# Optimization experiments

Hardware: AMD Instinct MI355X
Metric: run time of the kernel (lower is better)

## Reference

```python
import jax, jax.numpy as jnp
import numpy as np

WS = 8          # window_size
SHIFT = WS // 2 # shift for 'SW' type
HEADS = 6
HD = 32


def setup_inputs() -> dict:
    key = jax.random.key(0)
    ks = jax.random.split(key, 6)
    return {
        "x": jax.random.normal(ks[0], (4, 256, 256, 192), jnp.float32),
        "w_qkv": jax.random.normal(ks[1], (192, 576), jnp.float32) * 0.02,
        "b_qkv": jax.random.normal(ks[2], (576,), jnp.float32) * 0.02,
        "rel_pos": jax.random.normal(ks[3], (HEADS, 2 * WS - 1, 2 * WS - 1), jnp.float32) * 0.02,
        "w_out": jax.random.normal(ks[4], (192, 192), jnp.float32) * 0.02,
        "b_out": jax.random.normal(ks[5], (192,), jnp.float32) * 0.02,
    }


def reference(x, w_qkv, b_qkv, rel_pos, w_out, b_out):
    b, h, w, c = x.shape
    scale = HD ** (-0.5)
    wa = WS * WS  # window area
    # shifted-window roll
    x = jnp.roll(x, (-SHIFT, -SHIFT), axis=(1, 2))
    hw, ww = h // WS, w // WS
    nw = hw * ww
    # partition into windows: [b, nw, wa, c]
    xw = x.reshape(b, hw, WS, ww, WS, c).transpose(0, 1, 3, 2, 4, 5).reshape(b, nw, wa, c)
    qkv = xw @ w_qkv + b_qkv                       # [b, nw, wa, 3c]
    qkv = qkv.reshape(b, nw, wa, 3, HEADS, HD)
    q = qkv[..., 0, :, :] * scale
    k = qkv[..., 1, :, :]
    v = qkv[..., 2, :, :]
    attn = jnp.einsum('bnqhd,bnkhd->bnhqk', q, k)  # [b, nw, heads, wa, wa]
    # relative position bias
    coords = jnp.stack(jnp.meshgrid(jnp.arange(WS), jnp.arange(WS), indexing='ij')).reshape(2, -1).T  # [wa,2]
    rel = coords[:, None, :] - coords[None, :, :] + WS - 1   # [wa, wa, 2]
    bias = rel_pos[:, rel[..., 0], rel[..., 1]]              # [heads, wa, wa]
    attn = attn + bias[None, None]
    # shift mask (only last window masked, per the module's generate_mask)
    s = WS - SHIFT
    mask = jnp.zeros((nw, wa, wa), bool)
    mask = mask.at[-1, :s, s:].set(True).at[-1, s:, :s].set(True)
    attn = jnp.where(mask[None, :, None], -jnp.inf, attn)
    attn = jax.nn.softmax(attn, axis=-1)
    out = jnp.einsum('bnhqk,bnkhd->bnqhd', attn, v)          # [b, nw, wa, heads, hd]
    out = out.reshape(b, hw, ww, WS, WS, c).transpose(0, 1, 3, 2, 4, 5).reshape(b, h, w, c)
    out = out @ w_out + b_out
    out = jnp.roll(out, (SHIFT, SHIFT), axis=(1, 2))
    return out
```

## Files before the change

### kernel.cpp

```cpp
#include <hip/hip_runtime.h>
#include <hip/hip_bf16.h>

typedef __attribute__((ext_vector_type(8))) short short8;
typedef __attribute__((ext_vector_type(4))) float f32x4;
typedef __attribute__((ext_vector_type(4))) unsigned short u16x4;

#define MFMA(a, b, c) __builtin_amdgcn_mfma_f32_16x16x32_bf16((a), (b), (c), 0, 0, 0)

namespace {
constexpr int IMG = 256;
constexpr int NWIN = 1024;
constexpr float SCALE = 0.17677669529663687f;
constexpr float L2E   = 1.4426950408889634f;
}

__device__ __forceinline__ unsigned short f2bf1(float f) {
    __hip_bfloat16 h = __float2bfloat16(f);
    union { __hip_bfloat16 h; unsigned short u; } v; v.h = h;
    return v.u;
}
__device__ __forceinline__ unsigned pack2(float a, float b) {
    __hip_bfloat162 h = __float22bfloat162_rn(make_float2(a, b));
    union { __hip_bfloat162 h; unsigned u; } v; v.h = h;
    return v.u;
}
__device__ __forceinline__ float bf2f(unsigned short h) {
    union { unsigned u; float f; } v; v.u = ((unsigned)h) << 16;
    return v.f;
}

__global__ __launch_bounds__(256) void to_bf16_T(const float* __restrict__ in,
                                                 unsigned short* __restrict__ out,
                                                 int K, int N, int scale_n, float scale) {
    __shared__ float tile[32][65];
    const int t = threadIdx.x;
    const int nb = blockIdx.x * 64, kb = blockIdx.y * 32;
    const int tn = t & 63, tk = t >> 6;
#pragma unroll
    for (int p = 0; p < 8; ++p)
        tile[p * 4 + tk][tn] = in[(size_t)(kb + p * 4 + tk) * N + nb + tn];
    __syncthreads();
    const int n = t >> 2, kc = (t & 3) * 8;
    const float s = (nb + n) < scale_n ? scale : 1.0f;
    uint4 u;
    u.x = pack2(tile[kc + 0][n] * s, tile[kc + 1][n] * s);
    u.y = pack2(tile[kc + 2][n] * s, tile[kc + 3][n] * s);
    u.z = pack2(tile[kc + 4][n] * s, tile[kc + 5][n] * s);
    u.w = pack2(tile[kc + 6][n] * s, tile[kc + 7][n] * s);
    *(uint4*)(out + (size_t)(nb + n) * K + kb + kc) = u;
}

__global__ __launch_bounds__(256) void build_bias(const float* __restrict__ rel_pos,
                                                  const float* __restrict__ b_qkv,
                                                  unsigned short* __restrict__ bias3,
                                                  float* __restrict__ bq2) {
    const int o = blockIdx.x * 256 + threadIdx.x;
    const int k = o & 63, q = (o >> 6) & 63, h = o >> 12;
    const int qy = q >> 3, qx = q & 7, ky = k >> 3, kx = k & 7;
    const float bv = rel_pos[h * 225 + (qy - ky + 7) * 15 + (qx - kx + 7)] * L2E;
    bias3[o] = f2bf1(bv);
    const bool masked = (q < 4) != (k < 4);
    bias3[24576 + o] = masked ? f2bf1(-30000.0f) : f2bf1(bv);
    if (blockIdx.x == 0) {
        for (int i = threadIdx.x; i < 576; i += 256)
            bq2[i] = b_qkv[i] * (i < 192 ? SCALE : 1.0f);
    }
}

__global__ __launch_bounds__(256, 3)
void qkv_attn(const float* __restrict__ x,
              const float* __restrict__ bq2,
              const unsigned short* __restrict__ bias3,
              const unsigned short* __restrict__ wqT,
              unsigned short* __restrict__ oh_ws) {
    __shared__ unsigned short x_s[64][200];
    __shared__ unsigned short qp_s[64][72];
    __shared__ unsigned short kp_s[64][72];
    __shared__ unsigned short vT_s[64][72];

    const int tid = threadIdx.x;
    const int w   = tid >> 6;
    const int l   = tid & 63;
    const int l15 = l & 15, lg = l >> 4;
    const int wing = blockIdx.x;
    const int b   = wing >> 10;
    const int win = wing & (NWIN - 1);
    const int wy  = win >> 5, wx = win & 31;
    const unsigned short* bias_t = bias3 + ((win == NWIN - 1) ? 24576 : 0);

    {
        int t = tid / 48, r = tid % 48;
#pragma unroll
        for (int it = 0; it < 12; ++it) {
            const int pr = ((wy << 3) + (t >> 3) + 4) & (IMG - 1);
            const int pc = ((wx << 3) + (t & 7) + 4) & (IMG - 1);
            const float4 xv = *reinterpret_cast<const float4*>(
                x + ((size_t)((b * IMG + pr) * IMG + pc)) * 192 + r * 4);
            uint2 pk; pk.x = pack2(xv.x, xv.y); pk.y = pack2(xv.z, xv.w);
            *(uint2*)(&x_s[t][r * 4]) = pk;
            r += 16; t += 5;
            if (r >= 48) { r -= 48; t += 1; }
        }
    }
    __syncthreads();

    const int h_loc = w >> 1;
    const int qt0   = 2 * (w & 1);

#pragma unroll 1
    for (int g = 0; g < 3; ++g) {
        f32x4 aq[3][4];
#pragma unroll
        for (int ci = 0; ci < 3; ++ci) {
            const int t = w + 4 * ci;
            const int which = t >> 2, sub = t & 3;
            const int hh = sub >> 1, d0 = (sub & 1) * 16;
            f32x4 c0;
            if (which < 2) {
                const float4 b4 = *reinterpret_cast<const float4*>(
                    bq2 + which * 192 + (2 * g + hh) * 32 + d0 + 4 * lg);
                c0 = f32x4{b4.x, b4.y, b4.z, b4.w};
            } else {
                const float bb = bq2[384 + (2 * g + hh) * 32 + d0 + l15];
                c0 = f32x4{bb, bb, bb, bb};
            }
#pragma unroll
            for (int nt = 0; nt < 4; ++nt) aq[ci][nt] = c0;
        }

        __builtin_amdgcn_s_setprio(1);
#pragma unroll
        for (int ks = 0; ks < 6; ++ks) {
            short8 xf[4];
#pragma unroll
            for (int nt = 0; nt < 4; ++nt)
                xf[nt] = *(const short8*)(&x_s[16 * nt + l15][ks * 32 + lg * 8]);
#pragma unroll
            for (int ci = 0; ci < 3; ++ci) {
                const int t = w + 4 * ci;
                const int which = t >> 2, sub = t & 3;
                const int hh = sub >> 1, d0 = (sub & 1) * 16;
                const int grow = which * 192 + (2 * g + hh) * 32 + d0 + l15;
                const short8 wf = *(const short8*)(wqT + (size_t)grow * 192 + ks * 32 + lg * 8);
                if (which < 2) {
#pragma unroll
                    for (int nt = 0; nt < 4; ++nt) aq[ci][nt] = MFMA(wf, xf[nt], aq[ci][nt]);
                } else {
#pragma unroll
                    for (int nt = 0; nt < 4; ++nt) aq[ci][nt] = MFMA(xf[nt], wf, aq[ci][nt]);
                }
            }
        }
        __builtin_amdgcn_s_setprio(0);

#pragma unroll
        for (int ci = 0; ci < 3; ++ci) {
            const int t = w + 4 * ci;
            const int which = t >> 2, sub = t & 3;
            const int hh = sub >> 1, d0 = (sub & 1) * 16;
            if (which < 2) {
                const int rbase = hh * 32 + d0 + 4 * lg;
#pragma unroll
                for (int nt = 0; nt < 4; ++nt) {
                    const int tok = 16 * nt + l15;
                    uint2 pk;
                    pk.x = pack2(aq[ci][nt][0], aq[ci][nt][1]);
                    pk.y = pack2(aq[ci][nt][2], aq[ci][nt][3]);
                    if (which == 0) *(uint2*)(&qp_s[tok][rbase]) = pk;
                    else            *(uint2*)(&kp_s[tok][rbase]) = pk;
                }
            } else {
                const int dcol = hh * 32 + d0 + l15;
#pragma unroll
                for (int nt = 0; nt < 4; ++nt) {
                    uint2 pk;
                    pk.x = pack2(aq[ci][nt][0], aq[ci][nt][1]);
                    pk.y = pack2(aq[ci][nt][2], aq[ci][nt][3]);
                    *(uint2*)(&vT_s[dcol][16 * nt + 4 * lg]) = pk;
                }
            }
        }
        __syncthreads();

        short8 qf[2], kf[4];
#pragma unroll
        for (int mq = 0; mq < 2; ++mq)
            qf[mq] = *(const short8*)(&qp_s[16 * (qt0 + mq) + l15][h_loc * 32 + lg * 8]);
#pragma unroll
        for (int nt = 0; nt < 4; ++nt)
            kf[nt] = *(const short8*)(&kp_s[16 * nt + l15][h_loc * 32 + lg * 8]);
        f32x4 s[2][4];
        const f32x4 z = {0.f, 0.f, 0.f, 0.f};
#pragma unroll
        for (int mq = 0; mq < 2; ++mq)
#pragma unroll
            for (int nt = 0; nt < 4; ++nt) s[mq][nt] = MFMA(kf[nt], qf[mq], z);
        __syncthreads();

        unsigned short (*p_buf)[72] = (h_loc == 0) ? qp_s : kp_s;
        const int h = 2 * g + h_loc;
        float ri[2];
#pragma unroll
        for (int mq = 0; mq < 2; ++mq) {
            const int q = 16 * (qt0 + mq) + l15;
            float e[4][4], sum = 0.f;
#pragma unroll
            for (int nt = 0; nt < 4; ++nt) {
                const u16x4 bb = *(const u16x4*)(bias_t + (h * 64 + q) * 64 + 16 * nt + 4 * lg);
                float psum = 0.f;
#pragma unroll
                for (int j = 0; j < 4; ++j) {
                    e[nt][j] = __builtin_exp2f(fmaf(s[mq][nt][j], L2E, bf2f(bb[j])));
                    psum += e[nt][j];
                }
                sum += psum;
            }
            sum += __shfl_xor(sum, 16);
            sum += __shfl_xor(sum, 32);
            ri[mq] = __builtin_amdgcn_rcpf(sum);
#pragma unroll
            for (int nt = 0; nt < 4; ++nt) {
                uint2 pk;
                pk.x = pack2(e[nt][0], e[nt][1]);
                pk.y = pack2(e[nt][2], e[nt][3]);
                *(uint2*)(&p_buf[q][16 * nt + 4 * lg]) = pk;
            }
        }

        f32x4 o[2][2];
#pragma unroll
        for (int dm = 0; dm < 2; ++dm)
#pragma unroll
            for (int qn = 0; qn < 2; ++qn) o[dm][qn] = z;
#pragma unroll
        for (int ks2 = 0; ks2 < 2; ++ks2) {
            short8 pf[2];
#pragma unroll
            for (int qn = 0; qn < 2; ++qn)
                pf[qn] = *(const short8*)(&p_buf[16 * (qt0 + qn) + l15][ks2 * 32 + lg * 8]);
#pragma unroll
            for (int dm = 0; dm < 2; ++dm) {
                const short8 vf = *(const short8*)(&vT_s[h_loc * 32 + 16 * dm + l15][ks2 * 32 + lg * 8]);
#pragma unroll
                for (int qn = 0; qn < 2; ++qn) o[dm][qn] = MFMA(vf, pf[qn], o[dm][qn]);
            }
        }
#pragma unroll
        for (int dm = 0; dm < 2; ++dm)
#pragma unroll
            for (int qn = 0; qn < 2; ++qn) {
                const int tok = 16 * (qt0 + qn) + l15;
                const int c0 = h * 32 + 16 * dm + 4 * lg;
                const float rr = ri[qn];
                uint2 pk;
                pk.x = pack2(o[dm][qn][0] * rr, o[dm][qn][1] * rr);
                pk.y = pack2(o[dm][qn][2] * rr, o[dm][qn][3] * rr);
                *(uint2*)(oh_ws + (size_t)wing * 12288 + tok * 192 + c0) = pk;
            }
        if (g < 2) __syncthreads();
    }
}

__global__ __launch_bounds__(256, 6)
void gemm2_out(const unsigned short* __restrict__ oh_ws,
               const unsigned short* __restrict__ woT,
               const float* __restrict__ b_out,
               float* __restrict__ out) {
    __shared__ unsigned short oh_s[64][200];

    const int tid = threadIdx.x;
    const int w   = tid >> 6;
    const int l   = tid & 63;
    const int l15 = l & 15, lg = l >> 4;
    const int wing = blockIdx.x;
    const int b   = wing >> 10;
    const int win = wing & (NWIN - 1);
    const int wy  = win >> 5, wx = win & 31;

#pragma unroll
    for (int it = 0; it < 6; ++it) {
        const int i = tid + 256 * it;
        const int t = i / 24, c8 = i % 24;
        const uint4 u = *(const uint4*)(oh_ws + (size_t)wing * 12288 + t * 192 + c8 * 8);
        *(uint4*)(&oh_s[t][c8 * 8]) = u;
    }
    __syncthreads();

#pragma unroll
    for (int ci = 0; ci < 3; ++ci) {
        const int oc0 = 16 * (w + 4 * ci);
        const float4 bo = *reinterpret_cast<const float4*>(b_out + oc0 + 4 * lg);
        f32x4 acc[4];
#pragma unroll
        for (int nt = 0; nt < 4; ++nt) acc[nt] = f32x4{bo.x, bo.y, bo.z, bo.w};
#pragma unroll
        for (int ks = 0; ks < 6; ++ks) {
            const short8 af = *(const short8*)(woT + (size_t)(oc0 + l15) * 192 + ks * 32 + lg * 8);
#pragma unroll
            for (int nt = 0; nt < 4; ++nt) {
                const short8 bfr = *(const short8*)(&oh_s[16 * nt + l15][ks * 32 + lg * 8]);
                acc[nt] = MFMA(af, bfr, acc[nt]);
            }
        }
#pragma unroll
        for (int nt = 0; nt < 4; ++nt) {
            const int tok = 16 * nt + l15;
            const int pr = ((wy << 3) + (tok >> 3) + 4) & (IMG - 1);
            const int pc = ((wx << 3) + (tok & 7) + 4) & (IMG - 1);
            float* orow = out + (size_t)((b * IMG + pr) * IMG + pc) * 192;
            *reinterpret_cast<float4*>(orow + oc0 + 4 * lg) =
                make_float4(acc[nt][0], acc[nt][1], acc[nt][2], acc[nt][3]);
        }
    }
}

extern "C" void kernel_launch(void* const* d_in, const int* in_sizes, int n_in,
                              void* d_out, int out_size, void* d_ws, size_t ws_size,
                              hipStream_t stream) {
    (void)in_sizes; (void)n_in; (void)out_size; (void)ws_size;
    const float* x       = (const float*)d_in[0];
    const float* w_qkv   = (const float*)d_in[1];
    const float* b_qkv   = (const float*)d_in[2];
    const float* rel_pos = (const float*)d_in[3];
    const float* w_out   = (const float*)d_in[4];
    const float* b_out   = (const float*)d_in[5];
    float* out = (float*)d_out;

    unsigned short* wqT   = (unsigned short*)d_ws;
    unsigned short* woT   = wqT + 576 * 192;
    unsigned short* bias3 = woT + 192 * 192;
    float*          bq2   = (float*)(bias3 + 2 * 24576);
    unsigned short* oh_ws = (unsigned short*)(bq2 + 576);

    to_bf16_T<<<dim3(9, 6), 256, 0, stream>>>(w_qkv, wqT, 192, 576, 192, SCALE);
    to_bf16_T<<<dim3(3, 6), 256, 0, stream>>>(w_out, woT, 192, 192, 0, 1.0f);
    build_bias<<<dim3(96), 256, 0, stream>>>(rel_pos, b_qkv, bias3, bq2);

    qkv_attn<<<dim3(4 * NWIN), dim3(256), 0, stream>>>(x, bq2, bias3, wqT, oh_ws);
    gemm2_out<<<dim3(4 * NWIN), dim3(256), 0, stream>>>(oh_ws, woT, b_out, out);
}
```

Measured before the change: 314.9 us.

## Store softmax bias as fp32, simplify x load, hoist weight pointers, add MFMA priorities

```diff
diff --git a/kernel.cpp b/kernel.cpp
--- a/kernel.cpp
+++ b/kernel.cpp
@@ -3,7 +3,6 @@
 
 typedef __attribute__((ext_vector_type(8))) short short8;
 typedef __attribute__((ext_vector_type(4))) float f32x4;
-typedef __attribute__((ext_vector_type(4))) unsigned short u16x4;
 
 #define MFMA(a, b, c) __builtin_amdgcn_mfma_f32_16x16x32_bf16((a), (b), (c), 0, 0, 0)
 
@@ -14,19 +13,10 @@
 constexpr float L2E   = 1.4426950408889634f;
 }
 
-__device__ __forceinline__ unsigned short f2bf1(float f) {
-    __hip_bfloat16 h = __float2bfloat16(f);
-    union { __hip_bfloat16 h; unsigned short u; } v; v.h = h;
-    return v.u;
-}
 __device__ __forceinline__ unsigned pack2(float a, float b) {
     __hip_bfloat162 h = __float22bfloat162_rn(make_float2(a, b));
     union { __hip_bfloat162 h; unsigned u; } v; v.h = h;
     return v.u;
-}
-__device__ __forceinline__ float bf2f(unsigned short h) {
-    union { unsigned u; float f; } v; v.u = ((unsigned)h) << 16;
-    return v.f;
 }
 
 __global__ __launch_bounds__(256) void to_bf16_T(const float* __restrict__ in,
@@ -52,15 +42,15 @@
 
 __global__ __launch_bounds__(256) void build_bias(const float* __restrict__ rel_pos,
                                                   const float* __restrict__ b_qkv,
-                                                  unsigned short* __restrict__ bias3,
+                                                  float* __restrict__ biasf,
                                                   float* __restrict__ bq2) {
     const int o = blockIdx.x * 256 + threadIdx.x;
     const int k = o & 63, q = (o >> 6) & 63, h = o >> 12;
     const int qy = q >> 3, qx = q & 7, ky = k >> 3, kx = k & 7;
     const float bv = rel_pos[h * 225 + (qy - ky + 7) * 15 + (qx - kx + 7)] * L2E;
-    bias3[o] = f2bf1(bv);
+    biasf[o] = bv;
     const bool masked = (q < 4) != (k < 4);
-    bias3[24576 + o] = masked ? f2bf1(-30000.0f) : f2bf1(bv);
+    biasf[24576 + o] = masked ? -30000.0f : bv;
     if (blockIdx.x == 0) {
         for (int i = threadIdx.x; i < 576; i += 256)
             bq2[i] = b_qkv[i] * (i < 192 ? SCALE : 1.0f);
@@ -70,7 +60,7 @@
 __global__ __launch_bounds__(256, 3)
 void qkv_attn(const float* __restrict__ x,
               const float* __restrict__ bq2,
-              const unsigned short* __restrict__ bias3,
+              const float* __restrict__ biasf,
               const unsigned short* __restrict__ wqT,
               unsigned short* __restrict__ oh_ws) {
     __shared__ unsigned short x_s[64][200];
@@ -86,20 +76,20 @@
     const int b   = wing >> 10;
     const int win = wing & (NWIN - 1);
     const int wy  = win >> 5, wx = win & 31;
-    const unsigned short* bias_t = bias3 + ((win == NWIN - 1) ? 24576 : 0);
+    const float* bias_t = biasf + ((win == NWIN - 1) ? 24576 : 0);
 
     {
-        int t = tid / 48, r = tid % 48;
-#pragma unroll
-        for (int it = 0; it < 12; ++it) {
-            const int pr = ((wy << 3) + (t >> 3) + 4) & (IMG - 1);
-            const int pc = ((wx << 3) + (t & 7) + 4) & (IMG - 1);
-            const float4 xv = *reinterpret_cast<const float4*>(
-                x + ((size_t)((b * IMG + pr) * IMG + pc)) * 192 + r * 4);
+        const int t  = tid >> 2;
+        const int c0 = tid & 3;
+        const int pr = ((wy << 3) + (t >> 3) + 4) & (IMG - 1);
+        const int pc = ((wx << 3) + (t & 7) + 4) & (IMG - 1);
+        const float* xrow = x + ((size_t)((b * IMG + pr) * IMG + pc)) * 192;
+#pragma unroll
+        for (int i = 0; i < 12; ++i) {
+            const int c = c0 + 4 * i;
+            const float4 xv = *reinterpret_cast<const float4*>(xrow + c * 4);
             uint2 pk; pk.x = pack2(xv.x, xv.y); pk.y = pack2(xv.z, xv.w);
-            *(uint2*)(&x_s[t][r * 4]) = pk;
-            r += 16; t += 5;
-            if (r >= 48) { r -= 48; t += 1; }
+            *(uint2*)(&x_s[t][c * 4]) = pk;
         }
     }
     __syncthreads();
@@ -110,11 +100,14 @@
 #pragma unroll 1
     for (int g = 0; g < 3; ++g) {
         f32x4 aq[3][4];
+        const unsigned short* wp[3];
 #pragma unroll
         for (int ci = 0; ci < 3; ++ci) {
             const int t = w + 4 * ci;
             const int which = t >> 2, sub = t & 3;
             const int hh = sub >> 1, d0 = (sub & 1) * 16;
+            const int grow = which * 192 + (2 * g + hh) * 32 + d0 + l15;
+            wp[ci] = wqT + (size_t)grow * 192 + lg * 8;
             f32x4 c0;
             if (which < 2) {
                 const float4 b4 = *reinterpret_cast<const float4*>(
@@ -137,12 +130,9 @@
                 xf[nt] = *(const short8*)(&x_s[16 * nt + l15][ks * 32 + lg * 8]);
 #pragma unroll
             for (int ci = 0; ci < 3; ++ci) {
-                const int t = w + 4 * ci;
-                const int which = t >> 2, sub = t & 3;
-                const int hh = sub >> 1, d0 = (sub & 1) * 16;
-                const int grow = which * 192 + (2 * g + hh) * 32 + d0 + l15;
-                const short8 wf = *(const short8*)(wqT + (size_t)grow * 192 + ks * 32 + lg * 8);
-                if (which < 2) {
+                const short8 wf = *(const short8*)wp[ci];
+                wp[ci] += 32;
+                if (ci < 2 ? ((w + 4 * ci) >> 2) < 2 : ((w + 8) >> 2) < 2) {
 #pragma unroll
                     for (int nt = 0; nt < 4; ++nt) aq[ci][nt] = MFMA(wf, xf[nt], aq[ci][nt]);
                 } else {
@@ -191,10 +181,12 @@
             kf[nt] = *(const short8*)(&kp_s[16 * nt + l15][h_loc * 32 + lg * 8]);
         f32x4 s[2][4];
         const f32x4 z = {0.f, 0.f, 0.f, 0.f};
+        __builtin_amdgcn_s_setprio(1);
 #pragma unroll
         for (int mq = 0; mq < 2; ++mq)
 #pragma unroll
             for (int nt = 0; nt < 4; ++nt) s[mq][nt] = MFMA(kf[nt], qf[mq], z);
+        __builtin_amdgcn_s_setprio(0);
         __syncthreads();
 
         unsigned short (*p_buf)[72] = (h_loc == 0) ? qp_s : kp_s;
@@ -203,17 +195,16 @@
 #pragma unroll
         for (int mq = 0; mq < 2; ++mq) {
             const int q = 16 * (qt0 + mq) + l15;
+            const float* bq = bias_t + ((h * 64 + q) << 6) + 4 * lg;
             float e[4][4], sum = 0.f;
 #pragma unroll
             for (int nt = 0; nt < 4; ++nt) {
-                const u16x4 bb = *(const u16x4*)(bias_t + (h * 64 + q) * 64 + 16 * nt + 4 * lg);
-                float psum = 0.f;
-#pragma unroll
-                for (int j = 0; j < 4; ++j) {
-                    e[nt][j] = __builtin_exp2f(fmaf(s[mq][nt][j], L2E, bf2f(bb[j])));
-                    psum += e[nt][j];
-                }
-                sum += psum;
+                const float4 bb = *(const float4*)(bq + 16 * nt);
+                e[nt][0] = __builtin_exp2f(fmaf(s[mq][nt][0], L2E, bb.x));
+                e[nt][1] = __builtin_exp2f(fmaf(s[mq][nt][1], L2E, bb.y));
+                e[nt][2] = __builtin_exp2f(fmaf(s[mq][nt][2], L2E, bb.z));
+                e[nt][3] = __builtin_exp2f(fmaf(s[mq][nt][3], L2E, bb.w));
+                sum += (e[nt][0] + e[nt][1]) + (e[nt][2] + e[nt][3]);
             }
             sum += __shfl_xor(sum, 16);
             sum += __shfl_xor(sum, 32);
@@ -232,6 +223,7 @@
         for (int dm = 0; dm < 2; ++dm)
 #pragma unroll
             for (int qn = 0; qn < 2; ++qn) o[dm][qn] = z;
+        __builtin_amdgcn_s_setprio(1);
 #pragma unroll
         for (int ks2 = 0; ks2 < 2; ++ks2) {
             short8 pf[2];
@@ -245,6 +237,10 @@
                 for (int qn = 0; qn < 2; ++qn) o[dm][qn] = MFMA(vf, pf[qn], o[dm][qn]);
             }
         }
+        __builtin_amdgcn_s_setprio(0);
+
+        if (g < 2) __syncthreads();
+
 #pragma unroll
         for (int dm = 0; dm < 2; ++dm)
 #pragma unroll
@@ -257,7 +253,6 @@
                 pk.y = pack2(o[dm][qn][2] * rr, o[dm][qn][3] * rr);
                 *(uint2*)(oh_ws + (size_t)wing * 12288 + tok * 192 + c0) = pk;
             }
-        if (g < 2) __syncthreads();
     }
 }
 
@@ -328,14 +323,14 @@
 
     unsigned short* wqT   = (unsigned short*)d_ws;
     unsigned short* woT   = wqT + 576 * 192;
-    unsigned short* bias3 = woT + 192 * 192;
-    float*          bq2   = (float*)(bias3 + 2 * 24576);
+    float*          biasf = (float*)(woT + 192 * 192);
+    float*          bq2   = biasf + 2 * 24576;
     unsigned short* oh_ws = (unsigned short*)(bq2 + 576);
 
     to_bf16_T<<<dim3(9, 6), 256, 0, stream>>>(w_qkv, wqT, 192, 576, 192, SCALE);
     to_bf16_T<<<dim3(3, 6), 256, 0, stream>>>(w_out, woT, 192, 192, 0, 1.0f);
-    build_bias<<<dim3(96), 256, 0, stream>>>(rel_pos, b_qkv, bias3, bq2);
-
-    qkv_attn<<<dim3(4 * NWIN), dim3(256), 0, stream>>>(x, bq2, bias3, wqT, oh_ws);
+    build_bias<<<dim3(96), 256, 0, stream>>>(rel_pos, b_qkv, biasf, bq2);
+
+    qkv_attn<<<dim3(4 * NWIN), dim3(256), 0, stream>>>(x, bq2, biasf, wqT, oh_ws);
     gemm2_out<<<dim3(4 * NWIN), dim3(256), 0, stream>>>(oh_ws, woT, b_out, out);
 }
```

Result: no change. 314.7 us (-0.1%).
